# Optimization experiments

Measured on AMD Instinct MI355X. Metric: run time of the kernel, lower is better.

The kernel has to match this reference:

```python
import jax, jax.numpy as jnp
import numpy as np

DROPOUT_P = 0.1  # original source passed p=1 (degenerate, zeros output); 0.1 used for a meaningful baseline


def setup_inputs() -> dict:
    key0 = jax.random.key(0)
    ks = jax.random.split(key0, 11)
    B, H, L, D, DQK, DV = 2, 8, 2048, 1024, 64, 64
    return {
        "query": jax.random.normal(ks[0], (B, H, L, D), jnp.float32),
        "key":   jax.random.normal(ks[1], (B, H, L, D), jnp.float32),
        "value": jax.random.normal(ks[2], (B, H, L, D), jnp.float32),
        "Wq": jax.random.normal(ks[3], (D, DQK), jnp.float32) * (D ** -0.5),
        "bq": jax.random.normal(ks[4], (DQK,), jnp.float32) * 0.02,
        "Wk": jax.random.normal(ks[5], (D, DQK), jnp.float32) * (D ** -0.5),
        "bk": jax.random.normal(ks[6], (DQK,), jnp.float32) * 0.02,
        "Wv": jax.random.normal(ks[7], (D, DV), jnp.float32) * (D ** -0.5),
        "bv": jax.random.normal(ks[8], (DV,), jnp.float32) * 0.02,
        "Wo": jax.random.normal(ks[9], (DV, D), jnp.float32) * (DV ** -0.5),
        "bo": jax.random.normal(ks[10], (D,), jnp.float32) * 0.02,
    }


def reference(query, key, value, Wq, bq, Wk, bk, Wv, bv, Wo, bo):
    # Per-head linear projections on 4D inputs (B,H,L,d_model)
    q = query @ Wq + bq            # (B,H,Lq,dqk)
    k = key @ Wk + bk              # (B,H,Lk,dqk)
    v = value @ Wv + bv            # (B,H,Lk,dv)
    # Quirky scale from source: q.size(2)*q.size(3)/key.size(2) * key.size(-1)**-0.5
    dk = (q.shape[2] * q.shape[3] / key.shape[2]) * (key.shape[-1] ** -0.5)
    scores = jnp.einsum('bhqd,bhkd->bhqk', q, k) * jnp.float32(dk)
    attn = jax.nn.softmax(scores, axis=-1)
    # Deterministic dropout with fixed key (inverted-scale, matching F.dropout)
    keep = jax.random.bernoulli(jax.random.key(42), 1.0 - DROPOUT_P, attn.shape)
    attn = jnp.where(keep, attn / (1.0 - DROPOUT_P), jnp.float32(0.0))
    out = jnp.einsum('bhqk,bhkd->bhqd', attn, v)  # (B,H,Lq,dv)
    return out @ Wo + bo                           # (B,H,Lq,d_model)
```

## Files before the change

kernel.cpp:

```cpp
#include <hip/hip_runtime.h>
#include <stdint.h>

typedef _Float16 f16;
typedef __attribute__((ext_vector_type(8))) _Float16 f16x8;
typedef __attribute__((ext_vector_type(4))) float f32x4;

__device__ __forceinline__ uint32_t rotl1(uint32_t x, uint32_t n){
  return __builtin_amdgcn_alignbit(x, x, 32u - n);
}
__device__ __forceinline__ uint32_t tf_bits(uint32_t i){
  const uint32_t ks1 = 42u, ks2 = 0x1BD11BDAu ^ 42u;
  uint32_t x0 = 0u, x1 = i + 42u;
#define R4(a,b,c,d) \
  x0 += x1; x1 = rotl1(x1,a); x1 ^= x0; \
  x0 += x1; x1 = rotl1(x1,b); x1 ^= x0; \
  x0 += x1; x1 = rotl1(x1,c); x1 ^= x0; \
  x0 += x1; x1 = rotl1(x1,d); x1 ^= x0;
  R4(13,15,26,6)  x0 += ks1; x1 += ks2 + 1u;
  R4(17,29,16,24) x0 += ks2; x1 += 2u;
  R4(13,15,26,6)               x1 += ks1 + 3u;
  R4(17,29,16,24) x0 += ks1; x1 += ks2 + 4u;
  R4(13,15,26,6)  x0 += ks2; x1 += 5u;
#undef R4
  return x0 ^ x1;
}

__global__ __launch_bounds__(256) void wt_kernel(
    const float* __restrict__ Wq, const float* __restrict__ Wk,
    const float* __restrict__ Wv, const float* __restrict__ Wo,
    f16* __restrict__ WqT, f16* __restrict__ WkT,
    f16* __restrict__ WvT, f16* __restrict__ WoT)
{
  __shared__ __align__(16) f16 Tl[64][72];
  const int b = blockIdx.x, tid = threadIdx.x;
  const int which = b >> 4, t = b & 15;
  const float* src = which==0?Wq:(which==1?Wk:(which==2?Wv:Wo));
  const int rr = tid >> 2, cb = (tid & 3) * 16;
  if (which < 3){
    const float* s = src + (long)(t*64 + rr)*64 + cb;
    #pragma unroll
    for (int j=0;j<16;j++) Tl[cb+j][rr] = (f16)s[j];
  } else {
    const float* s = src + (long)rr*1024 + t*64 + cb;
    #pragma unroll
    for (int j=0;j<16;j++) Tl[cb+j][rr] = (f16)s[j];
  }
  __syncthreads();
  f16* dst = which==0?WqT:(which==1?WkT:(which==2?WvT:WoT));
  const int c = tid >> 2, kb = (tid & 3) * 16;
  if (which < 3){
    *(f16x8*)&dst[(long)c*1024 + t*64 + kb]     = *(const f16x8*)&Tl[c][kb];
    *(f16x8*)&dst[(long)c*1024 + t*64 + kb + 8] = *(const f16x8*)&Tl[c][kb+8];
  } else {
    *(f16x8*)&dst[(long)(t*64 + c)*64 + kb]     = *(const f16x8*)&Tl[c][kb];
    *(f16x8*)&dst[(long)(t*64 + c)*64 + kb + 8] = *(const f16x8*)&Tl[c][kb+8];
  }
}

__device__ __forceinline__ void proj_step(const float4* ab, const f16x8* wb, f32x4* acc){
  union { f16 h[8]; f16x8 v; } u0, u1;
  u0.h[0]=(f16)ab[0].x; u0.h[1]=(f16)ab[0].y; u0.h[2]=(f16)ab[0].z; u0.h[3]=(f16)ab[0].w;
  u0.h[4]=(f16)ab[1].x; u0.h[5]=(f16)ab[1].y; u0.h[6]=(f16)ab[1].z; u0.h[7]=(f16)ab[1].w;
  u1.h[0]=(f16)ab[2].x; u1.h[1]=(f16)ab[2].y; u1.h[2]=(f16)ab[2].z; u1.h[3]=(f16)ab[2].w;
  u1.h[4]=(f16)ab[3].x; u1.h[5]=(f16)ab[3].y; u1.h[6]=(f16)ab[3].z; u1.h[7]=(f16)ab[3].w;
  #pragma unroll
  for (int n=0;n<4;n++){
    acc[n] = __builtin_amdgcn_mfma_f32_16x16x32_f16(u0.v, wb[n*2],   acc[n], 0,0,0);
    acc[n] = __builtin_amdgcn_mfma_f32_16x16x32_f16(u1.v, wb[n*2+1], acc[n], 0,0,0);
  }
}

__global__ __launch_bounds__(256) void proj_kernel(
    const float* __restrict__ query, const float* __restrict__ keyp, const float* __restrict__ value,
    const f16* __restrict__ WqT, const f16* __restrict__ WkT, const f16* __restrict__ WvT,
    const float* __restrict__ bq, const float* __restrict__ bk, const float* __restrict__ bv,
    f16* __restrict__ qp, f16* __restrict__ kp, f16* __restrict__ vpT)
{
  const int bid = blockIdx.x;
  const int which = bid >> 9;
  const long m0 = (long)(bid & 511) * 64;
  const float* A    = which==0 ? query : (which==1 ? keyp : value);
  const f16*   WT   = which==0 ? WqT   : (which==1 ? WkT  : WvT);
  const float* bias = which==0 ? bq    : (which==1 ? bk   : bv);

  const int tid = threadIdx.x;
  const int lane = tid & 63, wave = tid >> 6;
  const int llo = lane & 15, lhi = lane >> 4;

  f32x4 acc[4];
  #pragma unroll
  for (int n=0;n<4;n++){
    float bb = bias[16*n + llo];
    acc[n][0]=bb; acc[n][1]=bb; acc[n][2]=bb; acc[n][3]=bb;
  }

  const float* arow = A + (m0 + wave*16 + llo)*1024 + lhi*8;
  const f16*   wrow = WT + (long)llo*1024 + lhi*8;

#define LOADA(k0, d) { \
    d[0] = *(const float4*)(arow + (k0)); \
    d[1] = *(const float4*)(arow + (k0) + 4); \
    d[2] = *(const float4*)(arow + (k0) + 32); \
    d[3] = *(const float4*)(arow + (k0) + 36); }
#define LOADW(k0, d) { \
    _Pragma("unroll") \
    for (int n=0;n<4;n++){ \
      d[n*2]   = *(const f16x8*)(wrow + n*16384 + (k0)); \
      d[n*2+1] = *(const f16x8*)(wrow + n*16384 + (k0) + 32); } }

  float4 a0[4], a1[4]; f16x8 w0[8], w1[8];
  LOADA(0, a0) LOADW(0, w0)
  #pragma unroll 1
  for (int it = 0; it < 16; it += 2){
    LOADA((it+1)*64, a1) LOADW((it+1)*64, w1)
    proj_step(a0, w0, acc);
    if (it + 2 < 16){ LOADA((it+2)*64, a0) LOADW((it+2)*64, w0) }
    proj_step(a1, w1, acc);
  }
#undef LOADA
#undef LOADW

  if (which < 2){
    const float scale = (which==0) ? 2.0f : 1.0f;
    f16* dst = (which==0) ? qp : kp;
    #pragma unroll
    for (int n=0;n<4;n++)
      #pragma unroll
      for (int j=0;j<4;j++){
        long row = m0 + wave*16 + lhi*4 + j;
        dst[row*64 + 16*n + llo] = (f16)(acc[n][j]*scale);
      }
  } else {
    long row0 = m0 + wave*16 + lhi*4;
    long bh = row0 >> 11;
    long lr = row0 & 2047;
    #pragma unroll
    for (int n=0;n<4;n++){
      union { f16 h[4]; ushort4 u; } pk;
      #pragma unroll
      for (int j=0;j<4;j++) pk.h[j] = (f16)acc[n][j];
      *(ushort4*)&vpT[(bh*64 + 16*n + llo)*2048 + lr] = pk.u;
    }
  }
}

__global__ __launch_bounds__(256) void flash_kernel(
    const f16* __restrict__ qp, const f16* __restrict__ kp, const f16* __restrict__ vpT,
    const f16* __restrict__ WoT, const float* __restrict__ bo, float* __restrict__ out)
{
  __shared__ __align__(16) f16 Klds[64][72];
  __shared__ __align__(16) f16 Vlds[64][72];
  __shared__ __align__(16) f16 Plds[4][16][72];
  __shared__ unsigned short Idl[4][1024];
  const int tid = threadIdx.x;
  const int lane = tid & 63, wave = tid >> 6;
  const int llo = lane & 15, lhi = lane >> 4;
  const int bh = blockIdx.y;
  const int q0 = blockIdx.x * 64;

  const f16* qbase = qp + ((long)bh*2048 + q0 + wave*16 + llo)*64 + lhi*8;
  f16x8 qf0 = *(const f16x8*)qbase;
  f16x8 qf1 = *(const f16x8*)(qbase + 32);

  f32x4 O[4];
  float mrun[4], lrun[4];
  #pragma unroll
  for (int n=0;n<4;n++){ O[n][0]=0.f;O[n][1]=0.f;O[n][2]=0.f;O[n][3]=0.f; }
  #pragma unroll
  for (int j=0;j<4;j++){ mrun[j] = -__builtin_inff(); lrun[j]=0.f; }

  const int sr = tid >> 2;
  const int sc = (tid & 3) * 16;
  const f16* kbh = kp + (long)bh*2048*64;
  const f16* vbh = vpT + (long)bh*64*2048;
  uint32_t base_w = (uint32_t)((bh*2048 + q0 + wave*16)*2048);

  for (int kv0 = 0; kv0 < 2048; kv0 += 64, base_w += 64u){
    {
      const f16* src = kbh + (long)(kv0 + sr)*64 + sc;
      f16x8 t0 = *(const f16x8*)src;
      f16x8 t1 = *(const f16x8*)(src+8);
      *(f16x8*)&Klds[sr][sc]   = t0;
      *(f16x8*)&Klds[sr][sc+8] = t1;
      const f16* vsrc = vbh + (long)sr*2048 + kv0 + sc;
      f16x8 u0 = *(const f16x8*)vsrc;
      f16x8 u1 = *(const f16x8*)(vsrc+8);
      *(f16x8*)&Vlds[sr][sc]   = u0;
      *(f16x8*)&Vlds[sr][sc+8] = u1;
    }
    __syncthreads();

    f32x4 s[4];
    #pragma unroll
    for (int n=0;n<4;n++){ s[n][0]=0.f;s[n][1]=0.f;s[n][2]=0.f;s[n][3]=0.f; }
    #pragma unroll
    for (int n=0;n<4;n++){
      f16x8 kf0 = *(const f16x8*)&Klds[16*n+llo][lhi*8];
      s[n] = __builtin_amdgcn_mfma_f32_16x16x32_f16(qf0, kf0, s[n], 0,0,0);
      f16x8 kf1 = *(const f16x8*)&Klds[16*n+llo][32+lhi*8];
      s[n] = __builtin_amdgcn_mfma_f32_16x16x32_f16(qf1, kf1, s[n], 0,0,0);
    }
    float pmax[4];
    #pragma unroll
    for (int j=0;j<4;j++)
      pmax[j] = fmaxf(fmaxf(s[0][j],s[1][j]), fmaxf(s[2][j],s[3][j]));
    #pragma unroll
    for (int off=1; off<16; off<<=1){
      #pragma unroll
      for (int j=0;j<4;j++) pmax[j] = fmaxf(pmax[j], __shfl_xor(pmax[j], off));
    }
    float esc[4];
    #pragma unroll
    for (int j=0;j<4;j++){
      float mnew = fmaxf(mrun[j], pmax[j]);
      esc[j] = __expf(mrun[j] - mnew);
      mrun[j] = mnew;
    }
    float p[4][4]; float lsum[4] = {0.f,0.f,0.f,0.f};
    #pragma unroll
    for (int n=0;n<4;n++)
      #pragma unroll
      for (int j=0;j<4;j++){
        p[n][j] = __expf(s[n][j] - mrun[j]);
        lsum[j] += p[n][j];
      }
    #pragma unroll
    for (int off=1; off<16; off<<=1){
      #pragma unroll
      for (int j=0;j<4;j++) lsum[j] += __shfl_xor(lsum[j], off);
    }
    #pragma unroll
    for (int j=0;j<4;j++) lrun[j] = lrun[j]*esc[j] + lsum[j];
    #pragma unroll
    for (int n=0;n<4;n++)
      #pragma unroll
      for (int j=0;j<4;j++) O[n][j] *= esc[j];

    uint32_t cnt = 0;
    #pragma unroll
    for (int j=0;j<4;j++){
      #pragma unroll
      for (int n=0;n<4;n++){
        float pm = p[n][j]*(1.0f/0.9f);
        bool surv = pm > 0x1.0p-25f;
        Plds[wave][lhi*4+j][16*n+llo] = (f16)pm;
        unsigned long long mk = __ballot(surv);
        if (mk){
          uint32_t pre = __builtin_amdgcn_mbcnt_hi((uint32_t)(mk>>32),
                         __builtin_amdgcn_mbcnt_lo((uint32_t)mk, 0u));
          if (surv)
            Idl[wave][cnt + pre] = (unsigned short)((j<<8)|(n<<6)|lane);
          cnt += (uint32_t)__builtin_popcountll(mk);
        }
      }
    }
    for (uint32_t pb = 0; pb < cnt; pb += 64){
      uint32_t idx = pb + (uint32_t)lane;
      if (idx < cnt){
        uint32_t id = (uint32_t)Idl[wave][idx];
        uint32_t jj = (id>>8)&3u, nn = (id>>6)&3u, ln = id & 63u;
        uint32_t i = base_w + (ln>>4)*8192u + jj*2048u + nn*16u + (ln&15u);
        uint32_t bits = tf_bits(i);
        if (bits >= 0xE6666600u)
          Plds[wave][(ln>>4)*4+jj][16*nn+(ln&15u)] = (f16)0;
      }
    }

    f16x8 pa0 = *(const f16x8*)&Plds[wave][llo][lhi*8];
    f16x8 pa1 = *(const f16x8*)&Plds[wave][llo][32+lhi*8];
    #pragma unroll
    for (int n=0;n<4;n++){
      f16x8 vf0 = *(const f16x8*)&Vlds[16*n+llo][lhi*8];
      O[n] = __builtin_amdgcn_mfma_f32_16x16x32_f16(pa0, vf0, O[n], 0,0,0);
      f16x8 vf1 = *(const f16x8*)&Vlds[16*n+llo][32+lhi*8];
      O[n] = __builtin_amdgcn_mfma_f32_16x16x32_f16(pa1, vf1, O[n], 0,0,0);
    }
    __syncthreads();
  }

  float rl[4];
  #pragma unroll
  for (int j=0;j<4;j++) rl[j] = 1.0f / lrun[j];
  #pragma unroll
  for (int n=0;n<4;n++)
    #pragma unroll
    for (int j=0;j<4;j++)
      Klds[wave*16 + lhi*4 + j][16*n + llo] = (f16)(O[n][j]*rl[j]);
  __syncthreads();

  f16x8 af0 = *(const f16x8*)&Klds[wave*16 + llo][lhi*8];
  f16x8 af1 = *(const f16x8*)&Klds[wave*16 + llo][32 + lhi*8];
  const long robase = (long)bh*2048 + q0 + wave*16 + lhi*4;
  for (int n0 = 0; n0 < 1024; n0 += 16){
    f16x8 b0 = *(const f16x8*)&WoT[(long)(n0+llo)*64 + lhi*8];
    f16x8 b1 = *(const f16x8*)&WoT[(long)(n0+llo)*64 + 32 + lhi*8];
    float bb = bo[n0+llo];
    f32x4 c; c[0]=bb; c[1]=bb; c[2]=bb; c[3]=bb;
    c = __builtin_amdgcn_mfma_f32_16x16x32_f16(af0, b0, c, 0,0,0);
    c = __builtin_amdgcn_mfma_f32_16x16x32_f16(af1, b1, c, 0,0,0);
    #pragma unroll
    for (int j=0;j<4;j++)
      out[(robase + j)*1024 + n0 + llo] = c[j];
  }
}

extern "C" void kernel_launch(void* const* d_in, const int* in_sizes, int n_in,
                              void* d_out, int out_size, void* d_ws, size_t ws_size,
                              hipStream_t stream){
  const float* query = (const float*)d_in[0];
  const float* key   = (const float*)d_in[1];
  const float* value = (const float*)d_in[2];
  const float* Wq = (const float*)d_in[3];
  const float* bq = (const float*)d_in[4];
  const float* Wk = (const float*)d_in[5];
  const float* bk = (const float*)d_in[6];
  const float* Wv = (const float*)d_in[7];
  const float* bv = (const float*)d_in[8];
  const float* Wo = (const float*)d_in[9];
  const float* bo = (const float*)d_in[10];
  float* out = (float*)d_out;

  char* ws = (char*)d_ws;
  f16* qp   = (f16*)(ws);
  f16* kp   = (f16*)(ws + ((size_t)4<<20));
  f16* vpT  = (f16*)(ws + ((size_t)8<<20));
  f16* WoT  = (f16*)(ws + ((size_t)20<<20));
  f16* WqT  = (f16*)(ws + ((size_t)21<<20));
  f16* WkT  = (f16*)(ws + ((size_t)21<<20) + (256<<10));
  f16* WvT  = (f16*)(ws + ((size_t)21<<20) + (512<<10));

  wt_kernel<<<dim3(64), dim3(256), 0, stream>>>(Wq,Wk,Wv,Wo,WqT,WkT,WvT,WoT);
  proj_kernel<<<dim3(1536), dim3(256), 0, stream>>>(
      query,key,value,WqT,WkT,WvT,bq,bk,bv,qp,kp,vpT);
  flash_kernel<<<dim3(32,16), dim3(256), 0, stream>>>(qp,kp,vpT,WoT,bo,out);
}
```

Baseline: 285.2 us.

## Stage projection A tiles through double-buffered LDS with coalesced row loads

```diff
diff --git a/kernel.cpp b/kernel.cpp
--- a/kernel.cpp
+++ b/kernel.cpp
@@ -57,25 +57,13 @@
   }
 }
 
-__device__ __forceinline__ void proj_step(const float4* ab, const f16x8* wb, f32x4* acc){
-  union { f16 h[8]; f16x8 v; } u0, u1;
-  u0.h[0]=(f16)ab[0].x; u0.h[1]=(f16)ab[0].y; u0.h[2]=(f16)ab[0].z; u0.h[3]=(f16)ab[0].w;
-  u0.h[4]=(f16)ab[1].x; u0.h[5]=(f16)ab[1].y; u0.h[6]=(f16)ab[1].z; u0.h[7]=(f16)ab[1].w;
-  u1.h[0]=(f16)ab[2].x; u1.h[1]=(f16)ab[2].y; u1.h[2]=(f16)ab[2].z; u1.h[3]=(f16)ab[2].w;
-  u1.h[4]=(f16)ab[3].x; u1.h[5]=(f16)ab[3].y; u1.h[6]=(f16)ab[3].z; u1.h[7]=(f16)ab[3].w;
-  #pragma unroll
-  for (int n=0;n<4;n++){
-    acc[n] = __builtin_amdgcn_mfma_f32_16x16x32_f16(u0.v, wb[n*2],   acc[n], 0,0,0);
-    acc[n] = __builtin_amdgcn_mfma_f32_16x16x32_f16(u1.v, wb[n*2+1], acc[n], 0,0,0);
-  }
-}
-
 __global__ __launch_bounds__(256) void proj_kernel(
     const float* __restrict__ query, const float* __restrict__ keyp, const float* __restrict__ value,
     const f16* __restrict__ WqT, const f16* __restrict__ WkT, const f16* __restrict__ WvT,
     const float* __restrict__ bq, const float* __restrict__ bk, const float* __restrict__ bv,
     f16* __restrict__ qp, f16* __restrict__ kp, f16* __restrict__ vpT)
 {
+  __shared__ __align__(16) f16 Alds[2][64][72];
   const int bid = blockIdx.x;
   const int which = bid >> 9;
   const long m0 = (long)(bid & 511) * 64;
@@ -94,31 +82,62 @@
     acc[n][0]=bb; acc[n][1]=bb; acc[n][2]=bb; acc[n][3]=bb;
   }
 
-  const float* arow = A + (m0 + wave*16 + llo)*1024 + lhi*8;
-  const f16*   wrow = WT + (long)llo*1024 + lhi*8;
-
-#define LOADA(k0, d) { \
-    d[0] = *(const float4*)(arow + (k0)); \
-    d[1] = *(const float4*)(arow + (k0) + 4); \
-    d[2] = *(const float4*)(arow + (k0) + 32); \
-    d[3] = *(const float4*)(arow + (k0) + 36); }
-#define LOADW(k0, d) { \
-    _Pragma("unroll") \
-    for (int n=0;n<4;n++){ \
-      d[n*2]   = *(const f16x8*)(wrow + n*16384 + (k0)); \
-      d[n*2+1] = *(const f16x8*)(wrow + n*16384 + (k0) + 32); } }
-
-  float4 a0[4], a1[4]; f16x8 w0[8], w1[8];
-  LOADA(0, a0) LOADW(0, w0)
+  const int ar = tid >> 2;
+  const int ac = (tid & 3) * 16;
+  const float* abase = A + (m0 + ar)*1024 + ac;
+  const f16* wbase = WT + (long)llo*1024 + lhi*8;
+
+  float4 st[4];
+  #pragma unroll
+  for (int q=0;q<4;q++) st[q] = *(const float4*)(abase + q*4);
+  {
+    union { f16 h[16]; f16x8 v[2]; } u;
+    #pragma unroll
+    for (int q=0;q<4;q++){
+      u.h[q*4+0]=(f16)st[q].x; u.h[q*4+1]=(f16)st[q].y;
+      u.h[q*4+2]=(f16)st[q].z; u.h[q*4+3]=(f16)st[q].w;
+    }
+    *(f16x8*)&Alds[0][ar][ac]   = u.v[0];
+    *(f16x8*)&Alds[0][ar][ac+8] = u.v[1];
+  }
+  __syncthreads();
+
+  int buf = 0;
   #pragma unroll 1
-  for (int it = 0; it < 16; it += 2){
-    LOADA((it+1)*64, a1) LOADW((it+1)*64, w1)
-    proj_step(a0, w0, acc);
-    if (it + 2 < 16){ LOADA((it+2)*64, a0) LOADW((it+2)*64, w0) }
-    proj_step(a1, w1, acc);
-  }
-#undef LOADA
-#undef LOADW
+  for (int t = 0; t < 16; ++t){
+    f16x8 wreg[8];
+    {
+      const f16* wk0 = wbase + t*64;
+      #pragma unroll
+      for (int n=0;n<4;n++){
+        wreg[n*2]   = *(const f16x8*)(wk0 + n*16384);
+        wreg[n*2+1] = *(const f16x8*)(wk0 + n*16384 + 32);
+      }
+    }
+    if (t < 15){
+      #pragma unroll
+      for (int q=0;q<4;q++) st[q] = *(const float4*)(abase + (t+1)*64 + q*4);
+    }
+    f16x8 af0 = *(const f16x8*)&Alds[buf][wave*16 + llo][lhi*8];
+    f16x8 af1 = *(const f16x8*)&Alds[buf][wave*16 + llo][32 + lhi*8];
+    #pragma unroll
+    for (int n=0;n<4;n++){
+      acc[n] = __builtin_amdgcn_mfma_f32_16x16x32_f16(af0, wreg[n*2],   acc[n], 0,0,0);
+      acc[n] = __builtin_amdgcn_mfma_f32_16x16x32_f16(af1, wreg[n*2+1], acc[n], 0,0,0);
+    }
+    if (t < 15){
+      union { f16 h[16]; f16x8 v[2]; } u;
+      #pragma unroll
+      for (int q=0;q<4;q++){
+        u.h[q*4+0]=(f16)st[q].x; u.h[q*4+1]=(f16)st[q].y;
+        u.h[q*4+2]=(f16)st[q].z; u.h[q*4+3]=(f16)st[q].w;
+      }
+      *(f16x8*)&Alds[buf^1][ar][ac]   = u.v[0];
+      *(f16x8*)&Alds[buf^1][ar][ac+8] = u.v[1];
+      __syncthreads();
+    }
+    buf ^= 1;
+  }
 
   if (which < 2){
     const float scale = (which==0) ? 2.0f : 1.0f;
```

After: 279.1 us. 2.1% less time.

## Coalesce projection input loads through LDS and pre-swizzle weights into MFMA fragment order

Applied to the files above, without the earlier changes.

```diff
diff --git a/kernel.cpp b/kernel.cpp
--- a/kernel.cpp
+++ b/kernel.cpp
@@ -28,59 +28,53 @@
 __global__ __launch_bounds__(256) void wt_kernel(
     const float* __restrict__ Wq, const float* __restrict__ Wk,
     const float* __restrict__ Wv, const float* __restrict__ Wo,
-    f16* __restrict__ WqT, f16* __restrict__ WkT,
-    f16* __restrict__ WvT, f16* __restrict__ WoT)
+    f16* __restrict__ WqF, f16* __restrict__ WkF,
+    f16* __restrict__ WvF, f16* __restrict__ WoT)
 {
-  __shared__ __align__(16) f16 Tl[64][72];
   const int b = blockIdx.x, tid = threadIdx.x;
   const int which = b >> 4, t = b & 15;
-  const float* src = which==0?Wq:(which==1?Wk:(which==2?Wv:Wo));
+  const int lane = tid & 63, wave = tid >> 6;
+
+  if (which < 3){
+    const float* W = which==0 ? Wq : (which==1 ? Wk : Wv);
+    f16* Wf        = which==0 ? WqF : (which==1 ? WkF : WvF);
+    const int lhi = lane >> 4, llo = lane & 15;
+    #pragma unroll
+    for (int ff = 0; ff < 2; ++ff){
+      const int f = wave + ff*4;
+      const int n = f >> 1, h = f & 1;
+      union { f16 h8[8]; f16x8 v; } pk;
+      #pragma unroll
+      for (int e = 0; e < 8; ++e)
+        pk.h8[e] = (f16)W[(long)(t*64 + h*32 + lhi*8 + e)*64 + n*16 + llo];
+      *(f16x8*)&Wf[((long)(t*8 + f)*64 + lane)*8] = pk.v;
+    }
+    return;
+  }
+
+  __shared__ __align__(16) f16 Tl[64][72];
   const int rr = tid >> 2, cb = (tid & 3) * 16;
-  if (which < 3){
-    const float* s = src + (long)(t*64 + rr)*64 + cb;
-    #pragma unroll
-    for (int j=0;j<16;j++) Tl[cb+j][rr] = (f16)s[j];
-  } else {
-    const float* s = src + (long)rr*1024 + t*64 + cb;
-    #pragma unroll
-    for (int j=0;j<16;j++) Tl[cb+j][rr] = (f16)s[j];
-  }
+  const float* s = Wo + (long)rr*1024 + t*64 + cb;
+  #pragma unroll
+  for (int j=0;j<16;j++) Tl[cb+j][rr] = (f16)s[j];
   __syncthreads();
-  f16* dst = which==0?WqT:(which==1?WkT:(which==2?WvT:WoT));
   const int c = tid >> 2, kb = (tid & 3) * 16;
-  if (which < 3){
-    *(f16x8*)&dst[(long)c*1024 + t*64 + kb]     = *(const f16x8*)&Tl[c][kb];
-    *(f16x8*)&dst[(long)c*1024 + t*64 + kb + 8] = *(const f16x8*)&Tl[c][kb+8];
-  } else {
-    *(f16x8*)&dst[(long)(t*64 + c)*64 + kb]     = *(const f16x8*)&Tl[c][kb];
-    *(f16x8*)&dst[(long)(t*64 + c)*64 + kb + 8] = *(const f16x8*)&Tl[c][kb+8];
-  }
-}
-
-__device__ __forceinline__ void proj_step(const float4* ab, const f16x8* wb, f32x4* acc){
-  union { f16 h[8]; f16x8 v; } u0, u1;
-  u0.h[0]=(f16)ab[0].x; u0.h[1]=(f16)ab[0].y; u0.h[2]=(f16)ab[0].z; u0.h[3]=(f16)ab[0].w;
-  u0.h[4]=(f16)ab[1].x; u0.h[5]=(f16)ab[1].y; u0.h[6]=(f16)ab[1].z; u0.h[7]=(f16)ab[1].w;
-  u1.h[0]=(f16)ab[2].x; u1.h[1]=(f16)ab[2].y; u1.h[2]=(f16)ab[2].z; u1.h[3]=(f16)ab[2].w;
-  u1.h[4]=(f16)ab[3].x; u1.h[5]=(f16)ab[3].y; u1.h[6]=(f16)ab[3].z; u1.h[7]=(f16)ab[3].w;
-  #pragma unroll
-  for (int n=0;n<4;n++){
-    acc[n] = __builtin_amdgcn_mfma_f32_16x16x32_f16(u0.v, wb[n*2],   acc[n], 0,0,0);
-    acc[n] = __builtin_amdgcn_mfma_f32_16x16x32_f16(u1.v, wb[n*2+1], acc[n], 0,0,0);
-  }
+  *(f16x8*)&WoT[(long)(t*64 + c)*64 + kb]     = *(const f16x8*)&Tl[c][kb];
+  *(f16x8*)&WoT[(long)(t*64 + c)*64 + kb + 8] = *(const f16x8*)&Tl[c][kb+8];
 }
 
 __global__ __launch_bounds__(256) void proj_kernel(
     const float* __restrict__ query, const float* __restrict__ keyp, const float* __restrict__ value,
-    const f16* __restrict__ WqT, const f16* __restrict__ WkT, const f16* __restrict__ WvT,
+    const f16* __restrict__ WqF, const f16* __restrict__ WkF, const f16* __restrict__ WvF,
     const float* __restrict__ bq, const float* __restrict__ bk, const float* __restrict__ bv,
     f16* __restrict__ qp, f16* __restrict__ kp, f16* __restrict__ vpT)
 {
+  __shared__ __align__(16) f16 Alds[2][64][72];
   const int bid = blockIdx.x;
   const int which = bid >> 9;
   const long m0 = (long)(bid & 511) * 64;
   const float* A    = which==0 ? query : (which==1 ? keyp : value);
-  const f16*   WT   = which==0 ? WqT   : (which==1 ? WkT  : WvT);
+  const f16*   WF   = which==0 ? WqF   : (which==1 ? WkF  : WvF);
   const float* bias = which==0 ? bq    : (which==1 ? bk   : bv);
 
   const int tid = threadIdx.x;
@@ -94,31 +88,46 @@
     acc[n][0]=bb; acc[n][1]=bb; acc[n][2]=bb; acc[n][3]=bb;
   }
 
-  const float* arow = A + (m0 + wave*16 + llo)*1024 + lhi*8;
-  const f16*   wrow = WT + (long)llo*1024 + lhi*8;
-
-#define LOADA(k0, d) { \
-    d[0] = *(const float4*)(arow + (k0)); \
-    d[1] = *(const float4*)(arow + (k0) + 4); \
-    d[2] = *(const float4*)(arow + (k0) + 32); \
-    d[3] = *(const float4*)(arow + (k0) + 36); }
-#define LOADW(k0, d) { \
+  const int rq = lane >> 4;
+  const int cf = (lane & 15) * 4;
+  const float* abase = A + (m0 + wave*16)*1024 + cf;
+  const f16* wbase = WF + (size_t)lane*8;
+
+#define LOADA(t, d) { _Pragma("unroll") \
+    for (int q=0;q<4;q++) d[q] = *(const float4*)(abase + (size_t)(q*4+rq)*1024 + (size_t)(t)*64); }
+#define STOREA(bf, d) { _Pragma("unroll") \
+    for (int q=0;q<4;q++){ \
+      union { f16 h[4]; unsigned long long u; } pk; \
+      pk.h[0]=(f16)d[q].x; pk.h[1]=(f16)d[q].y; pk.h[2]=(f16)d[q].z; pk.h[3]=(f16)d[q].w; \
+      *(unsigned long long*)&Alds[bf][wave*16 + q*4 + rq][cf] = pk.u; } }
+
+  float4 s0[4], s1[4];
+  LOADA(0, s0)
+  STOREA(0, s0)
+  LOADA(1, s1)
+
+#define PROJ_ITER(t, SLD, SST) { \
+    f16x8 wf[8]; \
+    _Pragma("unroll") \
+    for (int f=0; f<8; f++) wf[f] = *(const f16x8*)(wbase + (size_t)((t)*8+f)*512); \
+    if ((t) < 14) { LOADA((t)+2, SLD) } \
+    f16x8 af0 = *(const f16x8*)&Alds[(t)&1][wave*16 + llo][lhi*8]; \
+    f16x8 af1 = *(const f16x8*)&Alds[(t)&1][wave*16 + llo][32 + lhi*8]; \
     _Pragma("unroll") \
     for (int n=0;n<4;n++){ \
-      d[n*2]   = *(const f16x8*)(wrow + n*16384 + (k0)); \
-      d[n*2+1] = *(const f16x8*)(wrow + n*16384 + (k0) + 32); } }
-
-  float4 a0[4], a1[4]; f16x8 w0[8], w1[8];
-  LOADA(0, a0) LOADW(0, w0)
+      acc[n] = __builtin_amdgcn_mfma_f32_16x16x32_f16(af0, wf[n*2],   acc[n], 0,0,0); \
+      acc[n] = __builtin_amdgcn_mfma_f32_16x16x32_f16(af1, wf[n*2+1], acc[n], 0,0,0); \
+    } \
+    if ((t) < 15) { STOREA(((t)+1)&1, SST) } }
+
   #pragma unroll 1
-  for (int it = 0; it < 16; it += 2){
-    LOADA((it+1)*64, a1) LOADW((it+1)*64, w1)
-    proj_step(a0, w0, acc);
-    if (it + 2 < 16){ LOADA((it+2)*64, a0) LOADW((it+2)*64, w0) }
-    proj_step(a1, w1, acc);
-  }
+  for (int t = 0; t < 16; t += 2){
+    PROJ_ITER(t,   s0, s1)
+    PROJ_ITER(t+1, s1, s0)
+  }
+#undef PROJ_ITER
 #undef LOADA
-#undef LOADW
+#undef STOREA
 
   if (which < 2){
     const float scale = (which==0) ? 2.0f : 1.0f;
@@ -325,12 +334,12 @@
   f16* kp   = (f16*)(ws + ((size_t)4<<20));
   f16* vpT  = (f16*)(ws + ((size_t)8<<20));
   f16* WoT  = (f16*)(ws + ((size_t)20<<20));
-  f16* WqT  = (f16*)(ws + ((size_t)21<<20));
-  f16* WkT  = (f16*)(ws + ((size_t)21<<20) + (256<<10));
-  f16* WvT  = (f16*)(ws + ((size_t)21<<20) + (512<<10));
-
-  wt_kernel<<<dim3(64), dim3(256), 0, stream>>>(Wq,Wk,Wv,Wo,WqT,WkT,WvT,WoT);
+  f16* WqF  = (f16*)(ws + ((size_t)21<<20));
+  f16* WkF  = (f16*)(ws + ((size_t)21<<20) + (256<<10));
+  f16* WvF  = (f16*)(ws + ((size_t)21<<20) + (512<<10));
+
+  wt_kernel<<<dim3(64), dim3(256), 0, stream>>>(Wq,Wk,Wv,Wo,WqF,WkF,WvF,WoT);
   proj_kernel<<<dim3(1536), dim3(256), 0, stream>>>(
-      query,key,value,WqT,WkT,WvT,bq,bk,bv,qp,kp,vpT);
+      query,key,value,WqF,WkF,WvF,bq,bk,bv,qp,kp,vpT);
   flash_kernel<<<dim3(32,16), dim3(256), 0, stream>>>(qp,kp,vpT,WoT,bo,out);
 }
```

Measured after the change: 264.3 us. -7.3%, faster.
